# Optimization experiments

Measured on AMD Instinct MI355X. Metric: run time of the kernel, lower is better.

Reference implementation:

```python
import jax, jax.numpy as jnp
import numpy as np

N = 100_000      # nodes
E = 1_600_000    # edges (avg degree 16)
D_IN, D_H, D_OUT = 128, 128, 64


def setup_inputs() -> dict:
    key = jax.random.key(0)
    ks = jax.random.split(key, 6)
    x = jax.random.normal(ks[0], (N, D_IN), jnp.float32)
    edge_index = jax.random.randint(ks[1], (2, E), 0, N, dtype=jnp.int32)
    W1 = jax.random.normal(ks[2], (D_IN, D_H), jnp.float32) / np.sqrt(D_IN)
    b1 = jnp.zeros((D_H,), jnp.float32)
    W2 = jax.random.normal(ks[3], (D_H, D_OUT), jnp.float32) / np.sqrt(D_H)
    b2 = jnp.zeros((D_OUT,), jnp.float32)
    return {"x": x, "edge_index": edge_index, "W1": W1, "b1": b1, "W2": W2, "b2": b2}


def _gcn_layer(x, W, b, src, dst, n_nodes):
    # PyG GCNConv: h = x @ W; symmetric norm with self-loops; scatter-add; + bias
    h = x @ W                                        # [N, D_out]
    deg = jax.ops.segment_sum(jnp.ones_like(dst, jnp.float32), dst,
                              num_segments=n_nodes)  # self-loops => deg >= 1
    dinv = jax.lax.rsqrt(deg)                        # deg^{-1/2}
    norm = dinv[src] * dinv[dst]                     # [E+N]
    msg = h[src] * norm[:, None]                     # gather + scale
    out = jax.ops.segment_sum(msg, dst, num_segments=n_nodes)  # scatter-add
    return out + b


def reference(x, edge_index, W1, b1, W2, b2):
    n = x.shape[0]
    loop = jnp.arange(n, dtype=edge_index.dtype)
    src = jnp.concatenate([edge_index[0], loop])     # add self-loops
    dst = jnp.concatenate([edge_index[1], loop])
    h = _gcn_layer(x, W1, b1, src, dst, n)
    h = jax.nn.relu(h)
    # dropout(p=0.5) is identity in eval mode
    out = _gcn_layer(h, W2, b2, src, dst, n)
    return out
```

## Files before the change

kernel.cpp:

```cpp
#include <hip/hip_runtime.h>
#include <hip/hip_bf16.h>


#define NTHREADS 256
#define BSH 9
#define NBMAX 256

typedef unsigned int uint;
typedef unsigned short ushort;
typedef __attribute__((ext_vector_type(8))) short short8;
typedef __attribute__((ext_vector_type(4))) float floatx4;

__device__ __forceinline__ uint pack_bf16(float a, float b) {
    __hip_bfloat162 h = __float22bfloat162_rn(make_float2(a, b));
    return *reinterpret_cast<uint*>(&h);
}
__device__ __forceinline__ float bf16_lo(uint q) { return __uint_as_float(q << 16); }
__device__ __forceinline__ float bf16_hi(uint q) { return __uint_as_float(q & 0xffff0000u); }

__global__ __launch_bounds__(256) void bucket_hist_kernel(
    const int* __restrict__ dst, int* __restrict__ bcnt, int e, int nb) {
    __shared__ int hist[NBMAX];
    int t = threadIdx.x;
    for (int b = t; b < nb; b += 256) hist[b] = 0;
    __syncthreads();
    int e0 = blockIdx.x * 2048;
#pragma unroll
    for (int v = 0; v < 2; v++) {
        int gi = e0 + t * 8 + v * 4;
        if (gi + 3 < e) {
            int4 d4 = *(const int4*)&dst[gi];
            atomicAdd(&hist[d4.x >> BSH], 1);
            atomicAdd(&hist[d4.y >> BSH], 1);
            atomicAdd(&hist[d4.z >> BSH], 1);
            atomicAdd(&hist[d4.w >> BSH], 1);
        } else {
            for (int j = 0; j < 4; j++)
                if (gi + j < e) atomicAdd(&hist[dst[gi + j] >> BSH], 1);
        }
    }
    __syncthreads();
    for (int b = t; b < nb; b += 256) {
        int v = hist[b];
        if (v) atomicAdd(&bcnt[b], v);
    }
}

__global__ void bucket_scan(const int* __restrict__ bcnt, int* __restrict__ bstart,
                            int* __restrict__ bcursor, int nb) {
    __shared__ int buf[NBMAX];
    int t = threadIdx.x;
    int v = (t < nb) ? bcnt[t] : 0;
    buf[t] = v;
    __syncthreads();
    int x = v;
    for (int off = 1; off < NBMAX; off <<= 1) {
        int y = (t >= off) ? buf[t - off] : 0;
        __syncthreads();
        x += y;
        buf[t] = x;
        __syncthreads();
    }
    if (t < nb) {
        bstart[t] = x - v;
        bcursor[t] = x - v;
    }
}

__global__ __launch_bounds__(256) void partition_kernel(
    const int* __restrict__ src, const int* __restrict__ dst,
    int* __restrict__ bcursor, int2* __restrict__ staged, int e, int nb) {
    __shared__ int eS[2048];
    __shared__ int eD[2048];
    __shared__ int hist[NBMAX];
    __shared__ int base[NBMAX];
    int t = threadIdx.x;
    int e0 = blockIdx.x * 2048;

    for (int b = t; b < nb; b += 256) hist[b] = 0;
    __syncthreads();
#pragma unroll
    for (int v = 0; v < 2; v++) {
        int li = t * 8 + v * 4;
        int gi = e0 + li;
        int4 s4, d4;
        if (gi + 3 < e) {
            s4 = *(const int4*)&src[gi];
            d4 = *(const int4*)&dst[gi];
        } else {
            const int* sp = &src[gi];
            const int* dp = &dst[gi];
            s4.x = (gi + 0 < e) ? sp[0] : 0;  d4.x = (gi + 0 < e) ? dp[0] : -1;
            s4.y = (gi + 1 < e) ? sp[1] : 0;  d4.y = (gi + 1 < e) ? dp[1] : -1;
            s4.z = (gi + 2 < e) ? sp[2] : 0;  d4.z = (gi + 2 < e) ? dp[2] : -1;
            s4.w = (gi + 3 < e) ? sp[3] : 0;  d4.w = (gi + 3 < e) ? dp[3] : -1;
        }
        *(int4*)&eS[li] = s4;
        *(int4*)&eD[li] = d4;
        if (d4.x >= 0) atomicAdd(&hist[d4.x >> BSH], 1);
        if (d4.y >= 0) atomicAdd(&hist[d4.y >> BSH], 1);
        if (d4.z >= 0) atomicAdd(&hist[d4.z >> BSH], 1);
        if (d4.w >= 0) atomicAdd(&hist[d4.w >> BSH], 1);
    }
    __syncthreads();
    for (int b = t; b < nb; b += 256) {
        int v = hist[b];
        base[b] = v ? atomicAdd(&bcursor[b], v) : 0;
        hist[b] = 0;
    }
    __syncthreads();
#pragma unroll
    for (int i = 0; i < 8; i++) {
        int li = t + i * 256;
        int d = eD[li];
        if (d >= 0) {
            int b = d >> BSH;
            int r = atomicAdd(&hist[b], 1);
            staged[base[b] + r] = make_int2(eS[li], d);
        }
    }
}

__global__ __launch_bounds__(256) void fine_csr_kernel(
    const int2* __restrict__ staged, const int* __restrict__ bstart,
    const int* __restrict__ bcnt, int4* __restrict__ meta,
    float* __restrict__ dinv, int* __restrict__ rec, int n) {
    __shared__ int lcnt[512];
    __shared__ int tsum[256];
    int b = blockIdx.x;
    int t = threadIdx.x;
    lcnt[t] = 0;
    lcnt[t + 256] = 0;
    __syncthreads();
    int s0 = bstart[b];
    int m = bcnt[b];
    for (int i = t; i < m; i += 256)
        atomicAdd(&lcnt[staged[s0 + i].y & 511], 1);
    __syncthreads();
    int v0 = lcnt[2 * t];
    int v1 = lcnt[2 * t + 1];
    int tot = v0 + v1;
    tsum[t] = tot;
    __syncthreads();
    int x = tot;
    for (int off = 1; off < 256; off <<= 1) {
        int y = (t >= off) ? tsum[t - off] : 0;
        __syncthreads();
        x += y;
        tsum[t] = x;
        __syncthreads();
    }
    int excl = x - tot;
    int node = (b << BSH) + 2 * t;
    if (node < n) {
        float di = rsqrtf((float)v0 + 1.0f);
        dinv[node] = di;
        meta[node] = make_int4(s0 + excl, v0, __float_as_int(di), __float_as_int(di * di));
    }
    if (node + 1 < n) {
        float di = rsqrtf((float)v1 + 1.0f);
        dinv[node + 1] = di;
        meta[node + 1] = make_int4(s0 + excl + v0, v1, __float_as_int(di), __float_as_int(di * di));
    }
    lcnt[2 * t] = s0 + excl;
    lcnt[2 * t + 1] = s0 + excl + v0;
    __syncthreads();
    for (int i = t; i < m; i += 256) {
        int2 ed = staged[s0 + i];
        int li = ed.y & 511;
        int pos = atomicAdd(&lcnt[li], 1);
        rec[pos] = ed.x;
    }
}

template <int COLS, bool XF32>
__global__ __launch_bounds__(256) void gemm_mfma(const void* __restrict__ Xv,
                                                 const float* __restrict__ W,
                                                 uint* __restrict__ Cq,
                                                 const float* __restrict__ dscale,
                                                 int n) {
    __shared__ ushort sX[64 * 128];
    __shared__ ushort sWT[COLS * 128];
    int t = threadIdx.x;
    int rbase = blockIdx.x * 64;

    if (XF32) {
        const float* X = (const float*)Xv;
#pragma unroll
        for (int i = 0; i < 8; i++) {
            int f = t + 256 * i;
            int r = f >> 5;
            int c4 = f & 31;
            float4 v = make_float4(0.f, 0.f, 0.f, 0.f);
            int gr = rbase + r;
            if (gr < n) v = *(const float4*)(X + (size_t)gr * 128 + c4 * 4);
            uint lo = pack_bf16(v.x, v.y);
            uint hi = pack_bf16(v.z, v.w);
            int chunk = c4 >> 1;
            int sub = (c4 & 1) * 4;
            int off = r * 128 + (((chunk ^ (r & 15)) << 3) + sub);
            *(uint2*)&sX[off] = make_uint2(lo, hi);
        }
    } else {
        const ushort* X = (const ushort*)Xv;
#pragma unroll
        for (int i = 0; i < 4; i++) {
            int f = t + 256 * i;
            int r = f >> 4;
            int chunk = f & 15;
            uint4 v = make_uint4(0, 0, 0, 0);
            int gr = rbase + r;
            if (gr < n) v = *(const uint4*)(X + (size_t)gr * 128 + chunk * 8);
            int off = r * 128 + ((chunk ^ (r & 15)) << 3);
            *(uint4*)&sX[off] = v;
        }
    }
    {
        constexpr int UNITS = 64 * (COLS / 4);
        constexpr int PER_T = UNITS / 256;
#pragma unroll
        for (int i = 0; i < PER_T; i++) {
            int u = t + 256 * i;
            int kp = u / (COLS / 4);
            int n4 = u % (COLS / 4);
            int k = kp * 2;
            float4 w0 = *(const float4*)(W + (size_t)k * COLS + n4 * 4);
            float4 w1 = *(const float4*)(W + (size_t)(k + 1) * COLS + n4 * 4);
            int chunk = k >> 3;
            int sub = k & 7;
            const float* a0 = (const float*)&w0;
            const float* a1 = (const float*)&w1;
#pragma unroll
            for (int j = 0; j < 4; j++) {
                int nn = n4 * 4 + j;
                uint pk = pack_bf16(a0[j], a1[j]);
                int off = nn * 128 + (((chunk ^ (nn & 15)) << 3) + sub);
                *(uint*)&sWT[off] = pk;
            }
        }
    }
    __syncthreads();

    int lane = t & 63;
    int wave = t >> 6;
    int m = lane & 15;
    int q = lane >> 4;
    int r0 = wave * 16;

    floatx4 acc[COLS / 16];
#pragma unroll
    for (int c = 0; c < COLS / 16; c++) acc[c] = (floatx4){0.f, 0.f, 0.f, 0.f};

#pragma unroll
    for (int ks = 0; ks < 4; ks++) {
        int rr = r0 + m;
        int ca = (ks * 4 + q) ^ (rr & 15);
        short8 afrag = *(const short8*)&sX[rr * 128 + (ca << 3)];
#pragma unroll
        for (int c = 0; c < COLS / 16; c++) {
            int nn = c * 16 + m;
            int cb = (ks * 4 + q) ^ (nn & 15);
            short8 bfrag = *(const short8*)&sWT[nn * 128 + (cb << 3)];
            acc[c] = __builtin_amdgcn_mfma_f32_16x16x32_bf16(bfrag, afrag, acc[c], 0, 0, 0);
        }
    }

    int gr = rbase + r0 + m;
    if (gr < n) {
        float sc = dscale[gr];
#pragma unroll
        for (int c = 0; c < COLS / 16; c++) {
            uint2 pk;
            pk.x = pack_bf16(acc[c][0] * sc, acc[c][1] * sc);
            pk.y = pack_bf16(acc[c][2] * sc, acc[c][3] * sc);
            *(uint2*)&Cq[(size_t)gr * (COLS / 2) + c * 8 + q * 2] = pk;
        }
    }
}

__global__ __launch_bounds__(512) void agg128_mm64(
    const uint* __restrict__ hq, const int* __restrict__ rec,
    const int4* __restrict__ meta, const float* __restrict__ dinv,
    const float* __restrict__ bias, const float* __restrict__ W2,
    uint* __restrict__ h2q, int n) {
    __shared__ ushort sWT[64 * 128];
    __shared__ ushort sg[32 * 128];
    int t = threadIdx.x;

#pragma unroll
    for (int i = 0; i < 2; i++) {
        int u = t + 512 * i;
        int kp = u >> 4;
        int n4 = u & 15;
        int k = kp * 2;
        float4 w0 = *(const float4*)(W2 + (size_t)k * 64 + n4 * 4);
        float4 w1 = *(const float4*)(W2 + (size_t)(k + 1) * 64 + n4 * 4);
        int chunk = k >> 3;
        int sub = k & 7;
        const float* a0f = (const float*)&w0;
        const float* a1f = (const float*)&w1;
#pragma unroll
        for (int j = 0; j < 4; j++) {
            int nn = n4 * 4 + j;
            uint pk = pack_bf16(a0f[j], a1f[j]);
            *(uint*)&sWT[nn * 128 + (((chunk ^ (nn & 15)) << 3) + sub)] = pk;
        }
    }

    int qw = t >> 4;
    int fl = t & 15;
    int nb0 = blockIdx.x * 32;
    int w = nb0 + qw;
    bool valid = w < n;
    int wsafe = valid ? w : 0;
    const uint4* h4 = (const uint4*)hq;

    int4 mt = meta[wsafe];
    int j0 = mt.x;
    int deg = valid ? mt.y : 0;
    float di = __int_as_float(mt.z);

    uint4 qs = h4[(size_t)wsafe * 16 + fl];
    float a0 = bf16_lo(qs.x), a1 = bf16_hi(qs.x);
    float a2 = bf16_lo(qs.y), a3 = bf16_hi(qs.y);
    float a4 = bf16_lo(qs.z), a5 = bf16_hi(qs.z);
    float a6 = bf16_lo(qs.w), a7 = bf16_hi(qs.w);
    if (!valid) { a0 = a1 = a2 = a3 = a4 = a5 = a6 = a7 = 0.f; }

    const int* rp = rec + j0;
    int tt = 0;
    for (; tt + 8 <= deg; tt += 8) {
        int s[8]; uint4 q[8];
#pragma unroll
        for (int u = 0; u < 8; u++) s[u] = rp[tt + u];
#pragma unroll
        for (int u = 0; u < 8; u++) q[u] = h4[(size_t)s[u] * 16 + fl];
#pragma unroll
        for (int u = 0; u < 8; u++) {
            a0 += bf16_lo(q[u].x); a1 += bf16_hi(q[u].x);
            a2 += bf16_lo(q[u].y); a3 += bf16_hi(q[u].y);
            a4 += bf16_lo(q[u].z); a5 += bf16_hi(q[u].z);
            a6 += bf16_lo(q[u].w); a7 += bf16_hi(q[u].w);
        }
    }
    for (; tt + 2 <= deg; tt += 2) {
        int s0i = rp[tt], s1i = rp[tt + 1];
        uint4 q0 = h4[(size_t)s0i * 16 + fl];
        uint4 q1 = h4[(size_t)s1i * 16 + fl];
        a0 += bf16_lo(q0.x) + bf16_lo(q1.x);
        a1 += bf16_hi(q0.x) + bf16_hi(q1.x);
        a2 += bf16_lo(q0.y) + bf16_lo(q1.y);
        a3 += bf16_hi(q0.y) + bf16_hi(q1.y);
        a4 += bf16_lo(q0.z) + bf16_lo(q1.z);
        a5 += bf16_hi(q0.z) + bf16_hi(q1.z);
        a6 += bf16_lo(q0.w) + bf16_lo(q1.w);
        a7 += bf16_hi(q0.w) + bf16_hi(q1.w);
    }
    if (tt < deg) {
        int s = rp[tt];
        uint4 q0 = h4[(size_t)s * 16 + fl];
        a0 += bf16_lo(q0.x); a1 += bf16_hi(q0.x);
        a2 += bf16_lo(q0.y); a3 += bf16_hi(q0.y);
        a4 += bf16_lo(q0.z); a5 += bf16_hi(q0.z);
        a6 += bf16_lo(q0.w); a7 += bf16_hi(q0.w);
    }

    float4 bb0 = *(const float4*)&bias[8 * fl];
    float4 bb1 = *(const float4*)&bias[8 * fl + 4];
    uint4 pkv;
    pkv.x = pack_bf16(fmaxf(di * a0 + bb0.x, 0.f), fmaxf(di * a1 + bb0.y, 0.f));
    pkv.y = pack_bf16(fmaxf(di * a2 + bb0.z, 0.f), fmaxf(di * a3 + bb0.w, 0.f));
    pkv.z = pack_bf16(fmaxf(di * a4 + bb1.x, 0.f), fmaxf(di * a5 + bb1.y, 0.f));
    pkv.w = pack_bf16(fmaxf(di * a6 + bb1.z, 0.f), fmaxf(di * a7 + bb1.w, 0.f));
    *(uint4*)&sg[qw * 128 + ((fl ^ (qw & 15)) << 3)] = pkv;
    __syncthreads();

    int wave = t >> 6;
    int lane = t & 63;
    int m = lane & 15;
    int qq = lane >> 4;
    int rt = wave >> 2;
    int ct = wave & 3;
    floatx4 acc = (floatx4){0.f, 0.f, 0.f, 0.f};
#pragma unroll
    for (int ks = 0; ks < 4; ks++) {
        int rr = rt * 16 + m;
        int ca = (ks * 4 + qq) ^ (rr & 15);
        short8 afrag = *(const short8*)&sg[rr * 128 + (ca << 3)];
        int nn = ct * 16 + m;
        int cb = (ks * 4 + qq) ^ (nn & 15);
        short8 bfrag = *(const short8*)&sWT[nn * 128 + (cb << 3)];
        acc = __builtin_amdgcn_mfma_f32_16x16x32_bf16(bfrag, afrag, acc, 0, 0, 0);
    }
    int gr = nb0 + rt * 16 + m;
    if (gr < n) {
        float sc = dinv[gr];
        uint2 pk;
        pk.x = pack_bf16(acc[0] * sc, acc[1] * sc);
        pk.y = pack_bf16(acc[2] * sc, acc[3] * sc);
        *(uint2*)&h2q[(size_t)gr * 32 + ct * 8 + qq * 2] = pk;
    }
}

__global__ __launch_bounds__(256) void aggregate64q(
    const uint* __restrict__ hq, const int* __restrict__ rec,
    const int4* __restrict__ meta, const float* __restrict__ bias,
    float* __restrict__ out, int n) {
    int gt = blockIdx.x * 256 + threadIdx.x;
    int w = gt >> 3;
    if (w >= n) return;
    int fl = gt & 7;

    int4 mt = meta[w];
    int j0 = mt.x;
    int deg = mt.y;
    float di = __int_as_float(mt.z);
    const uint4* h4 = (const uint4*)hq;

    uint4 qs = h4[(size_t)w * 8 + fl];
    float a0 = bf16_lo(qs.x), a1 = bf16_hi(qs.x);
    float a2 = bf16_lo(qs.y), a3 = bf16_hi(qs.y);
    float a4 = bf16_lo(qs.z), a5 = bf16_hi(qs.z);
    float a6 = bf16_lo(qs.w), a7 = bf16_hi(qs.w);

    const int* rp = rec + j0;
    int tt = 0;
    for (; tt + 8 <= deg; tt += 8) {
        int s[8]; uint4 q[8];
#pragma unroll
        for (int u = 0; u < 8; u++) s[u] = rp[tt + u];
#pragma unroll
        for (int u = 0; u < 8; u++) q[u] = h4[(size_t)s[u] * 8 + fl];
#pragma unroll
        for (int u = 0; u < 8; u++) {
            a0 += bf16_lo(q[u].x); a1 += bf16_hi(q[u].x);
            a2 += bf16_lo(q[u].y); a3 += bf16_hi(q[u].y);
            a4 += bf16_lo(q[u].z); a5 += bf16_hi(q[u].z);
            a6 += bf16_lo(q[u].w); a7 += bf16_hi(q[u].w);
        }
    }
    for (; tt + 2 <= deg; tt += 2) {
        int s0i = rp[tt], s1i = rp[tt + 1];
        uint4 q0 = h4[(size_t)s0i * 8 + fl];
        uint4 q1 = h4[(size_t)s1i * 8 + fl];
        a0 += bf16_lo(q0.x) + bf16_lo(q1.x);
        a1 += bf16_hi(q0.x) + bf16_hi(q1.x);
        a2 += bf16_lo(q0.y) + bf16_lo(q1.y);
        a3 += bf16_hi(q0.y) + bf16_hi(q1.y);
        a4 += bf16_lo(q0.z) + bf16_lo(q1.z);
        a5 += bf16_hi(q0.z) + bf16_hi(q1.z);
        a6 += bf16_lo(q0.w) + bf16_lo(q1.w);
        a7 += bf16_hi(q0.w) + bf16_hi(q1.w);
    }
    if (tt < deg) {
        int s = rp[tt];
        uint4 q0 = h4[(size_t)s * 8 + fl];
        a0 += bf16_lo(q0.x); a1 += bf16_hi(q0.x);
        a2 += bf16_lo(q0.y); a3 += bf16_hi(q0.y);
        a4 += bf16_lo(q0.z); a5 += bf16_hi(q0.z);
        a6 += bf16_lo(q0.w); a7 += bf16_hi(q0.w);
    }

    float4 bb0 = *(const float4*)&bias[8 * fl];
    float4 bb1 = *(const float4*)&bias[8 * fl + 4];
    float4 o0, o1;
    o0.x = di * a0 + bb0.x; o0.y = di * a1 + bb0.y;
    o0.z = di * a2 + bb0.z; o0.w = di * a3 + bb0.w;
    o1.x = di * a4 + bb1.x; o1.y = di * a5 + bb1.y;
    o1.z = di * a6 + bb1.z; o1.w = di * a7 + bb1.w;
    *(float4*)&out[(size_t)w * 64 + 8 * fl] = o0;
    *(float4*)&out[(size_t)w * 64 + 8 * fl + 4] = o1;
}

extern "C" void kernel_launch(void* const* d_in, const int* in_sizes, int n_in,
                              void* d_out, int out_size, void* d_ws, size_t ws_size,
                              hipStream_t stream) {
    const float* x = (const float*)d_in[0];
    const int* edge = (const int*)d_in[1];
    const float* W1 = (const float*)d_in[2];
    const float* b1 = (const float*)d_in[3];
    const float* W2 = (const float*)d_in[4];
    const float* b2 = (const float*)d_in[5];

    const int N = in_sizes[0] / 128;
    const int E = in_sizes[1] / 2;
    const int* src = edge;
    const int* dst = edge + E;
    const int NB = (N + (1 << BSH) - 1) >> BSH;

    char* p = (char*)d_ws;
    int* bcnt = (int*)p;      p += NBMAX * 4;
    int* bstart = (int*)p;    p += NBMAX * 4;
    int* bcursor = (int*)p;   p += NBMAX * 4;
    float* dinv = (float*)p;  p += (size_t)N * 4;
    int4* meta = (int4*)p;    p += (size_t)N * 16;
    int* rec = (int*)p;       p += (size_t)E * 4;
    int2* staged = (int2*)p;  p += (size_t)E * 8;
    uint* hq = (uint*)p;      p += (size_t)N * 64 * 4;
    uint* h2q = (uint*)p;     p += (size_t)N * 32 * 4;

    float* out = (float*)d_out;
    const int eblocks = (E + 2047) / 2048;

    (void)hipMemsetAsync(bcnt, 0, NBMAX * 4, stream);
    bucket_hist_kernel<<<eblocks, 256, 0, stream>>>(dst, bcnt, E, NB);
    bucket_scan<<<1, NBMAX, 0, stream>>>(bcnt, bstart, bcursor, NB);
    partition_kernel<<<eblocks, 256, 0, stream>>>(src, dst, bcursor, staged, E, NB);
    fine_csr_kernel<<<NB, 256, 0, stream>>>(staged, bstart, bcnt, meta, dinv, rec, N);

    const int gblocks = (N + 63) / 64;

    gemm_mfma<128, true><<<gblocks, 256, 0, stream>>>(x, W1, hq, dinv, N);
    agg128_mm64<<<(N + 31) / 32, 512, 0, stream>>>(hq, rec, meta, dinv, b1, W2, h2q, N);
    aggregate64q<<<(N * 8 + 255) / 256, 256, 0, stream>>>(h2q, rec, meta, b2, out, N);
}
```

Measured before the change: 295.0 us.

## Pack staged edges into 32-bit words, use 256-node buckets, cache in LDS

```diff
diff --git a/kernel.cpp b/kernel.cpp
--- a/kernel.cpp
+++ b/kernel.cpp
@@ -3,8 +3,9 @@
 
 
 #define NTHREADS 256
-#define BSH 9
-#define NBMAX 256
+#define BSH 8
+#define NBMAX 512
+#define FC_CAP 8192
 
 typedef unsigned int uint;
 typedef unsigned short ushort;
@@ -69,9 +70,9 @@
 
 __global__ __launch_bounds__(256) void partition_kernel(
     const int* __restrict__ src, const int* __restrict__ dst,
-    int* __restrict__ bcursor, int2* __restrict__ staged, int e, int nb) {
-    __shared__ int eS[2048];
-    __shared__ int eD[2048];
+    int* __restrict__ bcursor, uint* __restrict__ staged, int e, int nb) {
+    __shared__ uint eP[2048];
+    __shared__ ushort eB[2048];
     __shared__ int hist[NBMAX];
     __shared__ int base[NBMAX];
     int t = threadIdx.x;
@@ -95,8 +96,16 @@
             s4.z = (gi + 2 < e) ? sp[2] : 0;  d4.z = (gi + 2 < e) ? dp[2] : -1;
             s4.w = (gi + 3 < e) ? sp[3] : 0;  d4.w = (gi + 3 < e) ? dp[3] : -1;
         }
-        *(int4*)&eS[li] = s4;
-        *(int4*)&eD[li] = d4;
+        uint4 p4;
+        p4.x = ((uint)s4.x << 8) | ((uint)d4.x & 255u);
+        p4.y = ((uint)s4.y << 8) | ((uint)d4.y & 255u);
+        p4.z = ((uint)s4.z << 8) | ((uint)d4.z & 255u);
+        p4.w = ((uint)s4.w << 8) | ((uint)d4.w & 255u);
+        *(uint4*)&eP[li] = p4;
+        eB[li + 0] = (d4.x >= 0) ? (ushort)(d4.x >> BSH) : (ushort)0xFFFF;
+        eB[li + 1] = (d4.y >= 0) ? (ushort)(d4.y >> BSH) : (ushort)0xFFFF;
+        eB[li + 2] = (d4.z >= 0) ? (ushort)(d4.z >> BSH) : (ushort)0xFFFF;
+        eB[li + 3] = (d4.w >= 0) ? (ushort)(d4.w >> BSH) : (ushort)0xFFFF;
         if (d4.x >= 0) atomicAdd(&hist[d4.x >> BSH], 1);
         if (d4.y >= 0) atomicAdd(&hist[d4.y >> BSH], 1);
         if (d4.z >= 0) atomicAdd(&hist[d4.z >> BSH], 1);
@@ -112,37 +121,37 @@
 #pragma unroll
     for (int i = 0; i < 8; i++) {
         int li = t + i * 256;
-        int d = eD[li];
-        if (d >= 0) {
-            int b = d >> BSH;
-            int r = atomicAdd(&hist[b], 1);
-            staged[base[b] + r] = make_int2(eS[li], d);
+        ushort bb = eB[li];
+        if (bb != (ushort)0xFFFF) {
+            int r = atomicAdd(&hist[bb], 1);
+            staged[base[bb] + r] = eP[li];
         }
     }
 }
 
 __global__ __launch_bounds__(256) void fine_csr_kernel(
-    const int2* __restrict__ staged, const int* __restrict__ bstart,
+    const uint* __restrict__ staged, const int* __restrict__ bstart,
     const int* __restrict__ bcnt, int4* __restrict__ meta,
     float* __restrict__ dinv, int* __restrict__ rec, int n) {
-    __shared__ int lcnt[512];
+    __shared__ uint eL[FC_CAP];
+    __shared__ int lcnt[256];
     __shared__ int tsum[256];
     int b = blockIdx.x;
     int t = threadIdx.x;
     lcnt[t] = 0;
-    lcnt[t + 256] = 0;
     __syncthreads();
     int s0 = bstart[b];
     int m = bcnt[b];
-    for (int i = t; i < m; i += 256)
-        atomicAdd(&lcnt[staged[s0 + i].y & 511], 1);
-    __syncthreads();
-    int v0 = lcnt[2 * t];
-    int v1 = lcnt[2 * t + 1];
-    int tot = v0 + v1;
-    tsum[t] = tot;
-    __syncthreads();
-    int x = tot;
+    for (int i = t; i < m; i += 256) {
+        uint pk = staged[s0 + i];
+        if (i < FC_CAP) eL[i] = pk;
+        atomicAdd(&lcnt[pk & 255u], 1);
+    }
+    __syncthreads();
+    int v = lcnt[t];
+    tsum[t] = v;
+    __syncthreads();
+    int x = v;
     for (int off = 1; off < 256; off <<= 1) {
         int y = (t >= off) ? tsum[t - off] : 0;
         __syncthreads();
@@ -150,26 +159,19 @@
         tsum[t] = x;
         __syncthreads();
     }
-    int excl = x - tot;
-    int node = (b << BSH) + 2 * t;
+    int excl = x - v;
+    int node = (b << BSH) + t;
     if (node < n) {
-        float di = rsqrtf((float)v0 + 1.0f);
+        float di = rsqrtf((float)v + 1.0f);
         dinv[node] = di;
-        meta[node] = make_int4(s0 + excl, v0, __float_as_int(di), __float_as_int(di * di));
-    }
-    if (node + 1 < n) {
-        float di = rsqrtf((float)v1 + 1.0f);
-        dinv[node + 1] = di;
-        meta[node + 1] = make_int4(s0 + excl + v0, v1, __float_as_int(di), __float_as_int(di * di));
-    }
-    lcnt[2 * t] = s0 + excl;
-    lcnt[2 * t + 1] = s0 + excl + v0;
+        meta[node] = make_int4(s0 + excl, v, __float_as_int(di), __float_as_int(di * di));
+    }
+    lcnt[t] = s0 + excl;
     __syncthreads();
     for (int i = t; i < m; i += 256) {
-        int2 ed = staged[s0 + i];
-        int li = ed.y & 511;
-        int pos = atomicAdd(&lcnt[li], 1);
-        rec[pos] = ed.x;
+        uint pk = (i < FC_CAP) ? eL[i] : staged[s0 + i];
+        int pos = atomicAdd(&lcnt[pk & 255u], 1);
+        rec[pos] = (int)(pk >> 8);
     }
 }
 
@@ -495,7 +497,7 @@
     float* dinv = (float*)p;  p += (size_t)N * 4;
     int4* meta = (int4*)p;    p += (size_t)N * 16;
     int* rec = (int*)p;       p += (size_t)E * 4;
-    int2* staged = (int2*)p;  p += (size_t)E * 8;
+    uint* staged = (uint*)p;  p += (size_t)E * 4;
     uint* hq = (uint*)p;      p += (size_t)N * 64 * 4;
     uint* h2q = (uint*)p;     p += (size_t)N * 32 * 4;
 
```

Measured after the change: 294.3 us. About the same (-0.3%).
